# Kernel tuning notes

Measured on AMD Instinct MI355X. Metric: run time of the kernel, lower is better.

Reference implementation:

```python
import jax, jax.numpy as jnp
import numpy as np

B, S, DIM = 4, 512, 2048
E, INTER = 32, 1024
G, TOPK_G, TOPK = 8, 4, 6
ROUTE_SCALE = 2.5
SHARED_INTER = 2 * INTER  # n_shared_experts * moe_inter_dim


def setup_inputs() -> dict:
    key = jax.random.key(0)
    ks = jax.random.split(key, 8)
    sd = 0.02
    return {
        "x": jax.random.normal(ks[0], (B, S, DIM), jnp.float32),
        "gate_w": jax.random.normal(ks[1], (E, DIM), jnp.float32) * sd,
        "w11": jax.random.normal(ks[2], (E, INTER, DIM), jnp.float32) * sd,  # gate proj (torch Linear weight [out,in])
        "w33": jax.random.normal(ks[3], (E, INTER, DIM), jnp.float32) * sd,  # up proj
        "w22": jax.random.normal(ks[4], (E, DIM, INTER), jnp.float32) * sd,  # down proj
        "sw1": jax.random.normal(ks[5], (SHARED_INTER, DIM), jnp.float32) * sd,
        "sw2": jax.random.normal(ks[6], (DIM, SHARED_INTER), jnp.float32) * sd,
        "sw3": jax.random.normal(ks[7], (SHARED_INTER, DIM), jnp.float32) * sd,
    }


def _gate(xf, gate_w):
    # sigmoid scores, group-limited greedy top-k (bias=None branch)
    scores = jax.nn.sigmoid(xf @ gate_w.T)                      # [T, E]
    gs = scores.reshape(-1, G, E // G)                          # [T, G, E/G]
    group_scores = gs.max(axis=-1)                              # amax since bias is None
    _, gidx = jax.lax.top_k(group_scores, TOPK_G)               # [T, TOPK_G]
    gmask = jnp.any(jnp.arange(G)[None, None, :] == gidx[:, :, None], axis=1)  # [T, G] keep-mask
    masked = jnp.where(gmask[:, :, None], gs, -jnp.inf).reshape(-1, E)
    _, idx = jax.lax.top_k(masked, TOPK)                        # [T, TOPK]
    w = jnp.take_along_axis(scores, idx, axis=1)                # gather from original (pre-mask) scores
    w = w / jnp.sum(w, axis=-1, keepdims=True) * ROUTE_SCALE    # sigmoid normalization + route_scale
    return w, idx


def reference(x, gate_w, w11, w33, w22, sw1, sw2, sw3):
    xf = x.reshape(-1, DIM)                                     # [T, D]
    T = xf.shape[0]
    w, idx = _gate(xf, gate_w)
    # dense combine weights: equals the gather->gmm->scatter*prob of the original
    c = jnp.zeros((T, E), xf.dtype).at[jnp.arange(T)[:, None], idx].add(w)  # [T, E]
    g = jnp.einsum('td,eid->tei', xf, w11)                      # fc1 (gate)
    u = jnp.einsum('td,eid->tei', xf, w33)                      # fc2 (up)
    act = jax.nn.silu(g) * u                                    # fused SiLU gating
    y = jnp.einsum('tei,te,edi->td', act, c, w22)               # down proj + weighted combine
    shared = (jax.nn.silu(xf @ sw1.T) * (xf @ sw3.T)) @ sw2.T   # shared experts MLP
    return (y + shared).reshape(x.shape)
```

## Files before the change

### kernel.cpp

```cpp
#include <hip/hip_runtime.h>
#include <hip/hip_bf16.h>

#define T_TOK  2048
#define DIMSZ  2048
#define NEXP   32
#define INTERS 1024
#define SINTER 2048
#define NTOPK  6

typedef __bf16 bf16x8 __attribute__((ext_vector_type(8)));
typedef float  f32x4  __attribute__((ext_vector_type(4)));
typedef unsigned short u16x8 __attribute__((ext_vector_type(8)));

__device__ __forceinline__ unsigned short f2b(float f) {
    __hip_bfloat16 h = __float2bfloat16(f);
    return __builtin_bit_cast(unsigned short, h);
}

__device__ __forceinline__ void gl_lds16(const unsigned short* g, unsigned short* l) {
    __builtin_amdgcn_global_load_lds(
        (const __attribute__((address_space(1))) void*)g,
        (__attribute__((address_space(3))) void*)l, 16, 0, 0);
}
__device__ __forceinline__ void gl_lds16f(const float* g, float* l) {
    __builtin_amdgcn_global_load_lds(
        (const __attribute__((address_space(1))) void*)g,
        (__attribute__((address_space(3))) void*)l, 16, 0, 0);
}

__device__ __forceinline__ bf16x8 cvt8(float4 lo, float4 hi) {
    u16x8 u;
    u[0] = f2b(lo.x); u[1] = f2b(lo.y); u[2] = f2b(lo.z); u[3] = f2b(lo.w);
    u[4] = f2b(hi.x); u[5] = f2b(hi.y); u[6] = f2b(hi.z); u[7] = f2b(hi.w);
    return __builtin_bit_cast(bf16x8, u);
}

__global__ void cvt_f2b(const float4* __restrict__ src, unsigned short* __restrict__ dst, int n8) {
    int stride = gridDim.x * blockDim.x;
    for (int i = blockIdx.x * blockDim.x + threadIdx.x; i < n8; i += stride) {
        float4 a = src[2 * (size_t)i];
        float4 b = src[2 * (size_t)i + 1];
        u16x8 o;
        o[0] = f2b(a.x); o[1] = f2b(a.y); o[2] = f2b(a.z); o[3] = f2b(a.w);
        o[4] = f2b(b.x); o[5] = f2b(b.y); o[6] = f2b(b.z); o[7] = f2b(b.w);
        *(u16x8*)&dst[(size_t)i * 8] = o;
    }
}

#define SCT 8
#define SCK 128
__global__ __launch_bounds__(256) void gate_scores_kernel(
    const float* __restrict__ x, const float* __restrict__ gw, float* __restrict__ scores)
{
    __shared__ float xs[SCT * SCK];
    __shared__ float gs[NEXP * (SCK + 1)];
    const int t0 = blockIdx.x * SCT;
    const int tid = threadIdx.x;
    const int tl = tid >> 5, e = tid & 31;
    float acc = 0.f;
    for (int k0 = 0; k0 < DIMSZ; k0 += SCK) {
        {
            int row = tid >> 5, d4 = tid & 31;
            *(float4*)&xs[row * SCK + d4 * 4] =
                *(const float4*)&x[(size_t)(t0 + row) * DIMSZ + k0 + d4 * 4];
        }
        #pragma unroll
        for (int i = 0; i < 4; ++i) {
            int lin = tid + i * 256;
            int row = lin >> 5, d4 = lin & 31;
            float4 v = *(const float4*)&gw[(size_t)row * DIMSZ + k0 + d4 * 4];
            float* dst = &gs[row * (SCK + 1) + d4 * 4];
            dst[0] = v.x; dst[1] = v.y; dst[2] = v.z; dst[3] = v.w;
        }
        __syncthreads();
        #pragma unroll 8
        for (int d = 0; d < SCK; ++d)
            acc += xs[tl * SCK + d] * gs[e * (SCK + 1) + d];
        __syncthreads();
    }
    scores[(size_t)(t0 + tl) * NEXP + e] = 1.f / (1.f + expf(-acc));
}

__global__ __launch_bounds__(256) void topk_kernel(
    const float* __restrict__ scores,
    int* __restrict__ counts, int* __restrict__ toklist, float* __restrict__ wgts)
{
    int t = blockIdx.x * 256 + threadIdx.x;
    if (t >= T_TOK) return;
    float sc[NEXP];
    #pragma unroll
    for (int e = 0; e < NEXP; ++e) sc[e] = scores[(size_t)t * NEXP + e];

    float gsc[8];
    #pragma unroll
    for (int g = 0; g < 8; ++g) {
        float m = sc[4 * g];
        #pragma unroll
        for (int j = 1; j < 4; ++j) m = fmaxf(m, sc[4 * g + j]);
        gsc[g] = m;
    }
    bool gsel[8] = {false, false, false, false, false, false, false, false};
    for (int it = 0; it < 4; ++it) {
        int bi = -1; float bv = -1e30f;
        #pragma unroll
        for (int g = 0; g < 8; ++g)
            if (!gsel[g] && gsc[g] > bv) { bv = gsc[g]; bi = g; }
        gsel[bi] = true;
    }
    bool esel[NEXP];
    #pragma unroll
    for (int e = 0; e < NEXP; ++e) esel[e] = false;
    int   idx[NTOPK];
    float w[NTOPK];
    float sum = 0.f;
    for (int it = 0; it < NTOPK; ++it) {
        int bi = -1; float bv = -1e30f;
        #pragma unroll
        for (int e = 0; e < NEXP; ++e) {
            if (!gsel[e >> 2] || esel[e]) continue;
            if (sc[e] > bv) { bv = sc[e]; bi = e; }
        }
        esel[bi] = true; idx[it] = bi; w[it] = bv; sum += bv;
    }
    float scale = 2.5f / sum;
    for (int k = 0; k < NTOPK; ++k) {
        int e = idx[k];
        int s = atomicAdd(&counts[e], 1);
        toklist[e * T_TOK + s] = (t << 3) | k;
        wgts[e * T_TOK + s]   = w[k] * scale;
    }
}

__device__ __forceinline__ void walk_experts(
    int ty, const int* __restrict__ counts, int& fe, int& fy, int& frb)
{
    int acc2 = 0, rb = 0;
    fe = -1; fy = 0; frb = 0;
    #pragma unroll
    for (int e2 = 0; e2 < NEXP; ++e2) {
        const int cnt = counts[e2];
        const int nt = (cnt + 127) >> 7;
        if (fe < 0 && ty < acc2 + nt) { fe = e2; fy = ty - acc2; frb = rb; }
        acc2 += nt; rb += cnt;
    }
}

__global__ __launch_bounds__(256, 3) void fc1_all(
    const unsigned short* __restrict__ A,
    const float* __restrict__ w11, const float* __restrict__ w33,
    const float* __restrict__ sw1, const float* __restrict__ sw3,
    unsigned short* __restrict__ h, unsigned short* __restrict__ hs,
    const int* __restrict__ counts, const int* __restrict__ toklist)
{
    constexpr int BK = 64, K = DIMSZ, NT = K / BK;
    __shared__ unsigned short As[128 * 64];
    __shared__ float B1s[64 * 64];
    __shared__ float B2s[64 * 64];

    const int tid = threadIdx.x;
    bool SH; int e, m0, n0, hbase = 0;
    {
        const int wgid = blockIdx.x;
        if (wgid < 512) {
            SH = true; e = NEXP; m0 = (wgid >> 5) * 128; n0 = (wgid & 31) * 64;
        } else {
            const int rid = wgid - 512;
            const int xt = rid & 15, ty = rid >> 4;
            int fe, fy, frb;
            walk_experts(ty, counts, fe, fy, frb);
            SH = false; e = fe; m0 = fy * 128; n0 = xt * 64; hbase = frb;
        }
    }
    if (!SH && e < 0) return;
    const int N = SH ? SINTER : INTERS;
    const int M = SH ? T_TOK : counts[e];

    const size_t eoff = SH ? 0 : (size_t)e * INTERS * DIMSZ;
    const float* B1 = (SH ? sw1 : w11) + eoff + (size_t)n0 * K;
    const float* B2 = (SH ? sw3 : w33) + eoff + (size_t)n0 * K;
    unsigned short* Hout = SH ? hs : h;

    const int wave = tid >> 6;
    const int lane = tid & 63;
    const int wm = (wave >> 1) * 64;
    const int wn = (wave & 1) * 32;
    const int lm = lane & 15;
    const int quad = lane >> 4;

    const unsigned short* aP[4];
    {
        const int l8 = lane >> 3;
        const int sg = (lane & 7) ^ l8;
        #pragma unroll
        for (int i = 0; i < 4; ++i) {
            const int row = (wave * 4 + i) * 8 + l8;
            const int gr = m0 + row;
            int ar;
            if (SH) ar = gr;
            else ar = (gr < M) ? (toklist[e * T_TOK + gr] >> 3) : 0;
            aP[i] = A + (size_t)ar * K + sg * 8;
        }
    }
    int offB[4];
    {
        #pragma unroll
        for (int i = 0; i < 4; ++i) {
            const int c = wave * 4 + i;
            const int row = 4 * c + (lane >> 4);
            const int g = (lane & 15) ^ (row & 7);
            offB[i] = row * K + g * 4;
        }
    }

    f32x4 acc1[4][2] = {};
    f32x4 acc2v[4][2] = {};

    for (int t = 0; t < NT; ++t) {
        const int k0 = t * BK;
        #pragma unroll
        for (int i = 0; i < 4; ++i)
            gl_lds16(aP[i] + k0, &As[(wave * 4 + i) * 512]);
        #pragma unroll
        for (int i = 0; i < 4; ++i) {
            gl_lds16f(B1 + offB[i] + k0, &B1s[(wave * 4 + i) * 256]);
            gl_lds16f(B2 + offB[i] + k0, &B2s[(wave * 4 + i) * 256]);
        }
        __syncthreads();

        #pragma unroll
        for (int kh = 0; kh < 2; ++kh) {
            const int soffA = (((kh << 2) | quad) ^ (lm & 7)) << 3;
            const int j0 = ((kh << 2) | quad) << 1;
            const int s0 = j0 ^ (lm & 7);
            const int s1 = (j0 | 1) ^ (lm & 7);
            bf16x8 af[4], bf1[2], bf2[2];
            #pragma unroll
            for (int ti = 0; ti < 4; ++ti)
                af[ti] = *(const bf16x8*)&As[(wm + ti * 16 + lm) * 64 + soffA];
            #pragma unroll
            for (int tj = 0; tj < 2; ++tj) {
                const int rB = (wn + tj * 16 + lm) * 64;
                bf1[tj] = cvt8(*(const float4*)&B1s[rB + s0 * 4],
                               *(const float4*)&B1s[rB + s1 * 4]);
                bf2[tj] = cvt8(*(const float4*)&B2s[rB + s0 * 4],
                               *(const float4*)&B2s[rB + s1 * 4]);
            }
            #pragma unroll
            for (int ti = 0; ti < 4; ++ti)
                #pragma unroll
                for (int tj = 0; tj < 2; ++tj) {
                    acc1[ti][tj] = __builtin_amdgcn_mfma_f32_16x16x32_bf16(
                        af[ti], bf1[tj], acc1[ti][tj], 0, 0, 0);
                    acc2v[ti][tj] = __builtin_amdgcn_mfma_f32_16x16x32_bf16(
                        af[ti], bf2[tj], acc2v[ti][tj], 0, 0, 0);
                }
        }
        __syncthreads();
    }

    #pragma unroll
    for (int ti = 0; ti < 4; ++ti) {
        #pragma unroll
        for (int r = 0; r < 4; ++r) {
            const int lrow = wm + ti * 16 + quad * 4 + r;
            const int grow = m0 + lrow;
            if (!SH && grow >= M) continue;
            const int cr = SH ? grow : (hbase + grow);
            #pragma unroll
            for (int tj = 0; tj < 2; ++tj) {
                int nn = n0 + wn + tj * 16 + lm;
                float g = acc1[ti][tj][r];
                float u = acc2v[ti][tj][r];
                float hv = g / (1.f + expf(-g)) * u;
                Hout[(size_t)cr * N + nn] = f2b(hv);
            }
        }
    }
}

template <int MODE>
__global__ __launch_bounds__(256, 3) void fc2_all(
    const unsigned short* __restrict__ h, const unsigned short* __restrict__ hs,
    const float* __restrict__ w22, const float* __restrict__ sw2,
    float* __restrict__ yexp, float* __restrict__ out,
    const int* __restrict__ counts, const int* __restrict__ toklist,
    const float* __restrict__ wgts)
{
    constexpr int BK = 32;
    __shared__ unsigned short As[128 * 32];
    __shared__ float Bs[128 * 32];

    const int tid = threadIdx.x;
    bool SH; int e, m0, n0, hbase = 0;
    {
        int wgid = blockIdx.x;
        if (MODE == 1) {
            SH = true; e = NEXP; m0 = (wgid >> 4) * 128; n0 = (wgid & 15) * 128;
        } else {
            if (MODE == 2) wgid += 256;
            if (wgid < 256) {
                SH = true; e = NEXP; m0 = (wgid >> 4) * 128; n0 = (wgid & 15) * 128;
            } else {
                const int rid = wgid - 256;
                const int xt = rid & 15, ty = rid >> 4;
                int fe, fy, frb;
                walk_experts(ty, counts, fe, fy, frb);
                SH = false; e = fe; m0 = fy * 128; n0 = xt * 128; hbase = frb;
            }
        }
    }
    if (!SH && e < 0) return;
    const int K = SH ? SINTER : INTERS;
    const int NT = K / BK;
    const int M = SH ? T_TOK : counts[e];
    if (m0 >= M) return;

    const unsigned short* Asrc = SH ? hs : h;
    const float* B = (SH ? sw2 : (w22 + (size_t)e * DIMSZ * INTERS)) + (size_t)n0 * K;
    float* C = SH ? out : ((MODE == 2) ? out : yexp);

    const int wave = tid >> 6;
    const int lane = tid & 63;
    const int wm = (wave >> 1) * 64;
    const int wn = (wave & 1) * 64;
    const int lm = lane & 15;
    const int quad = lane >> 4;

    const unsigned short* aP[2];
    {
        const int gs = (lane & 3) ^ ((lane >> 3) & 3);
        #pragma unroll
        for (int i = 0; i < 2; ++i) {
            const int row = (wave * 2 + i) * 16 + (lane >> 2);
            const int gr = m0 + row;
            int ar;
            if (SH) ar = gr;
            else ar = hbase + ((gr < M) ? gr : 0);
            aP[i] = Asrc + (size_t)ar * K + gs * 8;
        }
    }
    int offB[4];
    {
        const int gs = (lane & 7) ^ (lane >> 3);
        #pragma unroll
        for (int i = 0; i < 4; ++i) {
            const int row = (wave * 4 + i) * 8 + (lane >> 3);
            offB[i] = row * K + gs * 4;
        }
    }

    f32x4 acc[4][4] = {};

    const int ga = quad ^ ((lm >> 1) & 3);
    const int s0 = (quad << 1) ^ (lm & 7);
    const int s1 = s0 ^ 1;

    for (int t = 0; t < NT; ++t) {
        const int k0 = t * BK;
        #pragma unroll
        for (int i = 0; i < 2; ++i)
            gl_lds16(aP[i] + k0, &As[(wave * 2 + i) * 512]);
        #pragma unroll
        for (int i = 0; i < 4; ++i)
            gl_lds16f(B + offB[i] + k0, &Bs[(wave * 4 + i) * 256]);
        __syncthreads();

        bf16x8 af[4], bfr[4];
        #pragma unroll
        for (int ti = 0; ti < 4; ++ti)
            af[ti] = *(const bf16x8*)&As[(wm + ti * 16 + lm) * 32 + ga * 8];
        #pragma unroll
        for (int tj = 0; tj < 4; ++tj) {
            const int rB = (wn + tj * 16 + lm) * 32;
            bfr[tj] = cvt8(*(const float4*)&Bs[rB + s0 * 4],
                           *(const float4*)&Bs[rB + s1 * 4]);
        }
        #pragma unroll
        for (int ti = 0; ti < 4; ++ti)
            #pragma unroll
            for (int tj = 0; tj < 4; ++tj)
                acc[ti][tj] = __builtin_amdgcn_mfma_f32_16x16x32_bf16(
                    af[ti], bfr[tj], acc[ti][tj], 0, 0, 0);

        __syncthreads();
    }

    #pragma unroll
    for (int ti = 0; ti < 4; ++ti) {
        #pragma unroll
        for (int r = 0; r < 4; ++r) {
            const int lrow = wm + ti * 16 + quad * 4 + r;
            const int grow = m0 + lrow;
            int cr; float cw;
            if (SH) { cr = grow; cw = 1.f; }
            else {
                if (grow >= M) continue;
                int ent = toklist[e * T_TOK + grow];
                cr = (MODE == 2) ? (ent >> 3) : ((ent >> 3) * NTOPK + (ent & 7));
                cw = wgts[e * T_TOK + grow];
            }
            #pragma unroll
            for (int tj = 0; tj < 4; ++tj) {
                int nn = n0 + wn + tj * 16 + lm;
                float v = acc[ti][tj][r] * cw;
                if (MODE == 2 && !SH)
                    atomicAdd(&C[(size_t)cr * DIMSZ + nn], v);
                else
                    C[(size_t)cr * DIMSZ + nn] = v;
            }
        }
    }
}

__global__ __launch_bounds__(256) void combine_kernel(
    const float4* __restrict__ yexp, float4* __restrict__ out, int n4)
{
    const int D4 = DIMSZ / 4;
    int stride = gridDim.x * blockDim.x;
    for (int i = blockIdx.x * blockDim.x + threadIdx.x; i < n4; i += stride) {
        int t = i / D4, d4 = i - t * D4;
        const float4* r = yexp + (size_t)t * NTOPK * D4 + d4;
        float4 a = out[i];
        #pragma unroll
        for (int k = 0; k < NTOPK; ++k) {
            float4 s = r[(size_t)k * D4];
            a.x += s.x; a.y += s.y; a.z += s.z; a.w += s.w;
        }
        out[i] = a;
    }
}

extern "C" void kernel_launch(void* const* d_in, const int* in_sizes, int n_in,
                              void* d_out, int out_size, void* d_ws, size_t ws_size,
                              hipStream_t stream)
{
    const float* x   = (const float*)d_in[0];
    const float* gw  = (const float*)d_in[1];
    const float* w11 = (const float*)d_in[2];
    const float* w33 = (const float*)d_in[3];
    const float* w22 = (const float*)d_in[4];
    const float* sw1 = (const float*)d_in[5];
    const float* sw2 = (const float*)d_in[6];
    const float* sw3 = (const float*)d_in[7];
    float* out = (float*)d_out;

    char* ws = (char*)d_ws;
    size_t off = 0;
    auto alloc = [&](size_t b) { void* p = ws + off; off = (off + b + 255) & ~(size_t)255; return p; };
    int*            counts  = (int*)alloc(NEXP * 4);
    int*            toklist = (int*)alloc((size_t)NEXP * T_TOK * 4);
    float*          wgts    = (float*)alloc((size_t)NEXP * T_TOK * 4);
    float*          scores  = (float*)alloc((size_t)T_TOK * NEXP * 4);
    unsigned short* xb      = (unsigned short*)alloc((size_t)T_TOK * DIMSZ * 2);
    unsigned short* h       = (unsigned short*)alloc(((size_t)T_TOK * NTOPK + 128) * INTERS * 2);
    unsigned short* hs      = (unsigned short*)alloc((size_t)T_TOK * SINTER * 2);

    const size_t yBytes = (size_t)T_TOK * NTOPK * DIMSZ * 4;
    const bool DENSE = (off + yBytes + 256) <= ws_size;
    float* yexp = DENSE ? (float*)alloc(yBytes) : nullptr;

    hipMemsetAsync(counts, 0, NEXP * 4, stream);

    const int n4x = T_TOK * DIMSZ / 4;
    cvt_f2b<<<1024, 256, 0, stream>>>((const float4*)x, xb, T_TOK * DIMSZ / 8);

    gate_scores_kernel<<<T_TOK / SCT, 256, 0, stream>>>(x, gw, scores);
    topk_kernel<<<(T_TOK + 255) / 256, 256, 0, stream>>>(scores, counts, toklist, wgts);

    fc1_all<<<512 + 2048, 256, 0, stream>>>(
        xb, w11, w33, sw1, sw3, h, hs, counts, toklist);

    if (DENSE) {
        fc2_all<0><<<256 + 2048, 256, 0, stream>>>(
            h, hs, w22, sw2, yexp, out, counts, toklist, wgts);
        combine_kernel<<<2048, 256, 0, stream>>>((const float4*)yexp, (float4*)out, n4x);
    } else {
        fc2_all<1><<<256, 256, 0, stream>>>(
            h, hs, w22, sw2, nullptr, out, counts, toklist, wgts);
        fc2_all<2><<<2048, 256, 0, stream>>>(
            h, hs, w22, sw2, nullptr, out, counts, toklist, wgts);
    }
}
```

Before: 1.036 ms.

## Replace per-slot expert buffer and combine kernel with atomic accumulation into output

```diff
diff --git a/kernel.cpp b/kernel.cpp
--- a/kernel.cpp
+++ b/kernel.cpp
@@ -278,11 +278,10 @@
     }
 }
 
-template <int MODE>
 __global__ __launch_bounds__(256, 3) void fc2_all(
     const unsigned short* __restrict__ h, const unsigned short* __restrict__ hs,
     const float* __restrict__ w22, const float* __restrict__ sw2,
-    float* __restrict__ yexp, float* __restrict__ out,
+    float* __restrict__ out,
     const int* __restrict__ counts, const int* __restrict__ toklist,
     const float* __restrict__ wgts)
 {
@@ -293,20 +292,15 @@
     const int tid = threadIdx.x;
     bool SH; int e, m0, n0, hbase = 0;
     {
-        int wgid = blockIdx.x;
-        if (MODE == 1) {
+        const int wgid = blockIdx.x;
+        if (wgid < 256) {
             SH = true; e = NEXP; m0 = (wgid >> 4) * 128; n0 = (wgid & 15) * 128;
         } else {
-            if (MODE == 2) wgid += 256;
-            if (wgid < 256) {
-                SH = true; e = NEXP; m0 = (wgid >> 4) * 128; n0 = (wgid & 15) * 128;
-            } else {
-                const int rid = wgid - 256;
-                const int xt = rid & 15, ty = rid >> 4;
-                int fe, fy, frb;
-                walk_experts(ty, counts, fe, fy, frb);
-                SH = false; e = fe; m0 = fy * 128; n0 = xt * 128; hbase = frb;
-            }
+            const int rid = wgid - 256;
+            const int xt = rid & 15, ty = rid >> 4;
+            int fe, fy, frb;
+            walk_experts(ty, counts, fe, fy, frb);
+            SH = false; e = fe; m0 = fy * 128; n0 = xt * 128; hbase = frb;
         }
     }
     if (!SH && e < 0) return;
@@ -317,7 +311,6 @@
 
     const unsigned short* Asrc = SH ? hs : h;
     const float* B = (SH ? sw2 : (w22 + (size_t)e * DIMSZ * INTERS)) + (size_t)n0 * K;
-    float* C = SH ? out : ((MODE == 2) ? out : yexp);
 
     const int wave = tid >> 6;
     const int lane = tid & 63;
@@ -396,37 +389,15 @@
             else {
                 if (grow >= M) continue;
                 int ent = toklist[e * T_TOK + grow];
-                cr = (MODE == 2) ? (ent >> 3) : ((ent >> 3) * NTOPK + (ent & 7));
+                cr = ent >> 3;
                 cw = wgts[e * T_TOK + grow];
             }
             #pragma unroll
             for (int tj = 0; tj < 4; ++tj) {
                 int nn = n0 + wn + tj * 16 + lm;
-                float v = acc[ti][tj][r] * cw;
-                if (MODE == 2 && !SH)
-                    atomicAdd(&C[(size_t)cr * DIMSZ + nn], v);
-                else
-                    C[(size_t)cr * DIMSZ + nn] = v;
+                atomicAdd(&out[(size_t)cr * DIMSZ + nn], acc[ti][tj][r] * cw);
             }
         }
-    }
-}
-
-__global__ __launch_bounds__(256) void combine_kernel(
-    const float4* __restrict__ yexp, float4* __restrict__ out, int n4)
-{
-    const int D4 = DIMSZ / 4;
-    int stride = gridDim.x * blockDim.x;
-    for (int i = blockIdx.x * blockDim.x + threadIdx.x; i < n4; i += stride) {
-        int t = i / D4, d4 = i - t * D4;
-        const float4* r = yexp + (size_t)t * NTOPK * D4 + d4;
-        float4 a = out[i];
-        #pragma unroll
-        for (int k = 0; k < NTOPK; ++k) {
-            float4 s = r[(size_t)k * D4];
-            a.x += s.x; a.y += s.y; a.z += s.z; a.w += s.w;
-        }
-        out[i] = a;
     }
 }
 
@@ -455,13 +426,9 @@
     unsigned short* h       = (unsigned short*)alloc(((size_t)T_TOK * NTOPK + 128) * INTERS * 2);
     unsigned short* hs      = (unsigned short*)alloc((size_t)T_TOK * SINTER * 2);
 
-    const size_t yBytes = (size_t)T_TOK * NTOPK * DIMSZ * 4;
-    const bool DENSE = (off + yBytes + 256) <= ws_size;
-    float* yexp = DENSE ? (float*)alloc(yBytes) : nullptr;
-
     hipMemsetAsync(counts, 0, NEXP * 4, stream);
-
-    const int n4x = T_TOK * DIMSZ / 4;
+    hipMemsetAsync(out, 0, out_size, stream);
+
     cvt_f2b<<<1024, 256, 0, stream>>>((const float4*)x, xb, T_TOK * DIMSZ / 8);
 
     gate_scores_kernel<<<T_TOK / SCT, 256, 0, stream>>>(x, gw, scores);
@@ -470,14 +437,6 @@
     fc1_all<<<512 + 2048, 256, 0, stream>>>(
         xb, w11, w33, sw1, sw3, h, hs, counts, toklist);
 
-    if (DENSE) {
-        fc2_all<0><<<256 + 2048, 256, 0, stream>>>(
-            h, hs, w22, sw2, yexp, out, counts, toklist, wgts);
-        combine_kernel<<<2048, 256, 0, stream>>>((const float4*)yexp, (float4*)out, n4x);
-    } else {
-        fc2_all<1><<<256, 256, 0, stream>>>(
-            h, hs, w22, sw2, nullptr, out, counts, toklist, wgts);
-        fc2_all<2><<<2048, 256, 0, stream>>>(
-            h, hs, w22, sw2, nullptr, out, counts, toklist, wgts);
-    }
-}
+    fc2_all<<<256 + 2048, 256, 0, stream>>>(
+        h, hs, w22, sw2, out, counts, toklist, wgts);
+}
```

Result: no change. 1.040 ms (+0.4%).
